# Performance work log

Measured on AMD Instinct MI355X. Metric: run time of the kernel, lower is better.

## Reference

```python
import jax, jax.numpy as jnp
import numpy as np

K = 3
PAD = 1
HEADS = 8
DIM = 256
HEAD_DIM = DIM // HEADS
SCALE = HEAD_DIM ** -0.5
B, IN_C, H, W = 1, 256, 40, 40
DN = ('NCHW', 'OIHW', 'NCHW')


def conv3(x, w):
    return jax.lax.conv_general_dilated(x, w, (1, 1), [(PAD, PAD), (PAD, PAD)], dimension_numbers=DN)


def cbr(x, w, s, b):
    # Conv (no bias) + eval-mode BatchNorm folded into per-channel scale/shift + ReLU
    y = conv3(x, w)
    return jax.nn.relu(y * s[None, :, None, None] + b[None, :, None, None])


def unfold(x):
    # [B,C,H,W] -> [B, C*K*K, H, W]; channels ordered (C, kh, kw), matching torch nn.Unfold
    return jax.lax.conv_general_dilated_patches(x, (K, K), (1, 1), [(PAD, PAD), (PAD, PAD)], dimension_numbers=DN)


def fold(p, h, w):
    # p: [B, C, K, K, h, w]; overlap-add (stride 1), matching F.fold
    b, c = p.shape[:2]
    out = jnp.zeros((b, c, h + 2 * PAD, w + 2 * PAD), p.dtype)
    for i in range(K):
        for j in range(K):
            out = out.at[:, :, i:i + h, j:j + w].add(p[:, :, i, j])
    return out[:, :, PAD:PAD + h, PAD:PAD + w]


def attn_pass(feat_hwc, v_chw, Wa, ba, Wp, bp):
    b, h, w, _ = feat_hwc.shape
    L = h * w
    # unfolded values: [B, heads, L, k^2, head_dim]
    vu = unfold(v_chw).reshape(b, HEADS, HEAD_DIM, K * K, L).transpose(0, 1, 4, 3, 2)
    # attention logits predicted from fg/bg features: [B, heads, L, k^2, k^2]
    logits = (feat_hwc @ Wa + ba).reshape(b, L, HEADS, K * K, K * K).transpose(0, 2, 1, 3, 4) * SCALE
    attn = jax.nn.softmax(logits, axis=-1)
    xw = jnp.einsum('bnlpq,bnlqd->bnlpd', attn, vu)
    # -> [B, dim*k^2, L] layout (C outer, then k^2), reshaped for fold
    xw = xw.transpose(0, 1, 4, 3, 2).reshape(b, DIM, K, K, h, w)
    y = fold(xw, h, w)  # [B, dim, h, w]
    return y.transpose(0, 2, 3, 1) @ Wp + bp  # proj, BHWC


def reference(x, fg, bg, Wc1, s1, b1, Wc2, s2, b2, Wv, bv, Wfg, bfg, Wbg, bbg, Wp, bp, Wc3, s3, b3, Wc4, s4, b4):
    h0 = cbr(cbr(x, Wc1, s1, b1), Wc2, s2, b2)  # input_cbr -> [B, dim, H, W]
    xh = h0.transpose(0, 2, 3, 1)               # BHWC
    v = (xh @ Wv + bv).transpose(0, 3, 1, 2)    # [B, dim, H, W]
    x1 = attn_pass(fg.transpose(0, 2, 3, 1), v, Wfg, bfg, Wp, bp)                            # fg pass, BHWC
    x2 = attn_pass(bg.transpose(0, 2, 3, 1), x1.transpose(0, 3, 1, 2), Wbg, bbg, Wp, bp)     # bg pass, BHWC
    return cbr(cbr(x2.transpose(0, 3, 1, 2), Wc3, s3, b3), Wc4, s4, b4)


def setup_inputs() -> dict:
    key = jax.random.key(0)
    ks = jax.random.split(key, 20)
    def rn(k, shape, s=0.02):
        return jax.random.normal(k, shape, jnp.float32) * s
    A = K ** 4 * HEADS  # 648
    ones = jnp.ones((DIM,), jnp.float32)
    return {
        'x': jax.random.normal(ks[0], (B, IN_C, H, W), jnp.float32),
        'fg': jax.random.normal(ks[1], (B, DIM, H, W), jnp.float32),
        'bg': jax.random.normal(ks[2], (B, DIM, H, W), jnp.float32),
        'Wc1': rn(ks[3], (DIM, IN_C, 3, 3)), 's1': ones, 'b1': rn(ks[4], (DIM,)),
        'Wc2': rn(ks[5], (DIM, DIM, 3, 3)), 's2': ones, 'b2': rn(ks[6], (DIM,)),
        'Wv': rn(ks[7], (DIM, DIM)), 'bv': rn(ks[8], (DIM,)),
        'Wfg': rn(ks[9], (DIM, A)), 'bfg': rn(ks[10], (A,)),
        'Wbg': rn(ks[11], (DIM, A)), 'bbg': rn(ks[12], (A,)),
        'Wp': rn(ks[13], (DIM, DIM)), 'bp': rn(ks[14], (DIM,)),
        'Wc3': rn(ks[15], (DIM, DIM, 3, 3)), 's3': ones, 'b3': rn(ks[16], (DIM,)),
        'Wc4': rn(ks[17], (DIM, DIM, 3, 3)), 's4': ones, 'b4': rn(ks[18], (DIM,)),
    }
```

## Files before the change

kernel.cpp:

```cpp
#include <hip/hip_runtime.h>
#include <hip/hip_bf16.h>

namespace {
constexpr int kHW   = 40;
constexpr int kNPIX = kHW * kHW;
constexpr int kDIM  = 256;
constexpr int kPADW = 42;
constexpr int kACOL = 648;
constexpr float kSCALE = 0.17677669529663687f;
}

using bf16 = __hip_bfloat16;
typedef __attribute__((ext_vector_type(8))) short sh8;
typedef __attribute__((ext_vector_type(4))) float f32x4;

static __device__ __forceinline__ bf16 f2bf(float f)  { return __float2bfloat16(f); }
static __device__ __forceinline__ float bf2f(bf16 b)  { return __bfloat162float(b); }

__global__ __launch_bounds__(256) void prep_all(
    const float* __restrict__ Wc1, const float* __restrict__ Wc2,
    const float* __restrict__ Wc3, const float* __restrict__ Wc4,
    const float* __restrict__ Wfg, const float* __restrict__ Wbg,
    const float* __restrict__ Wv,  const float* __restrict__ Wp,
    const float* __restrict__ x,   const float* __restrict__ fg,
    const float* __restrict__ bg,
    bf16* __restrict__ Wt1, bf16* __restrict__ Wt2,
    bf16* __restrict__ Wt3, bf16* __restrict__ Wt4,
    bf16* __restrict__ WaTf, bf16* __restrict__ WaTb,
    bf16* __restrict__ WvT, bf16* __restrict__ WpT,
    bf16* __restrict__ SHf, bf16* __restrict__ SHb,
    bf16* __restrict__ Pb0, bf16* __restrict__ Pb1) {
  __shared__ float smem[2304];
  int b = blockIdx.x, t = threadIdx.x;

  if (b < 1024) {
    int w = b >> 8, oc = b & 255;
    const float* src = (w == 0) ? Wc1 : (w == 1) ? Wc2 : (w == 2) ? Wc3 : Wc4;
    bf16* dst        = (w == 0) ? Wt1 : (w == 1) ? Wt2 : (w == 2) ? Wt3 : Wt4;
    src += (size_t)oc * 2304;
    for (int i = t; i < 2304; i += 256) smem[i] = src[i];
    __syncthreads();
#pragma unroll
    for (int tap = 0; tap < 9; ++tap)
      dst[(size_t)(tap * 256 + oc) * 256 + t] = f2bf(smem[t * 9 + tap]);
    return;
  }

  float (*tile)[33] = (float(*)[33])smem;
  int tx = t & 31, ty = t >> 5;

  if (b < 1360) {
    int b2 = b - 1024;
    const float* in = (b2 < 168) ? Wfg : Wbg;
    bf16* outp      = (b2 < 168) ? WaTf : WaTb;
    int rb = b2 % 168;
    int bx = rb % 21, by = rb / 21;
    int c0 = bx * 32, r0 = by * 32;
#pragma unroll
    for (int rr = ty; rr < 32; rr += 8) {
      int c = c0 + tx;
      tile[rr][tx] = (c < kACOL) ? in[(size_t)(r0 + rr) * kACOL + c] : 0.f;
    }
    __syncthreads();
#pragma unroll
    for (int rr = ty; rr < 32; rr += 8)
      outp[(size_t)(c0 + rr) * 256 + r0 + tx] = f2bf(tile[tx][rr]);
    return;
  }

  if (b < 1488) {
    int b3 = b - 1360;
    const float* in = (b3 < 64) ? Wv : Wp;
    bf16* outp      = (b3 < 64) ? WvT : WpT;
    int rb = b3 & 63;
    int bx = rb & 7, by = rb >> 3;
    int c0 = bx * 32, r0 = by * 32;
#pragma unroll
    for (int rr = ty; rr < 32; rr += 8)
      tile[rr][tx] = in[(size_t)(r0 + rr) * 256 + c0 + tx];
    __syncthreads();
#pragma unroll
    for (int rr = ty; rr < 32; rr += 8)
      outp[(size_t)(c0 + rr) * 256 + r0 + tx] = f2bf(tile[tx][rr]);
    return;
  }

  if (b < 2288) {
    int b4 = b - 1488;
    const float* in = (b4 < 400) ? fg : bg;
    bf16* outp      = (b4 < 400) ? SHf : SHb;
    int rb = b4 % 400;
    int bx = rb % 50, by = rb / 50;
    int c0 = bx * 32, r0 = by * 32;
#pragma unroll
    for (int rr = ty; rr < 32; rr += 8)
      tile[rr][tx] = in[(size_t)(r0 + rr) * kNPIX + c0 + tx];
    __syncthreads();
#pragma unroll
    for (int rr = ty; rr < 32; rr += 8)
      outp[(size_t)(c0 + rr) * 256 + r0 + tx] = f2bf(tile[tx][rr]);
    return;
  }

  if (b < 2688) {
    int b5 = b - 2288;
    int bx = b5 % 50, by = b5 / 50;
    int c0 = bx * 32, r0 = by * 32;
#pragma unroll
    for (int rr = ty; rr < 32; rr += 8)
      tile[rr][tx] = x[(size_t)(r0 + rr) * kNPIX + c0 + tx];
    __syncthreads();
#pragma unroll
    for (int rr = ty; rr < 32; rr += 8) {
      int l = c0 + rr;
      int yy = l / kHW, xx = l % kHW;
      Pb0[(size_t)((yy + 1) * kPADW + xx + 1) * kDIM + r0 + tx] = f2bf(tile[tx][rr]);
    }
    return;
  }

  {
    int k = b - 2688;
    int py, px;
    if (k < 42)      { py = 0;         px = k; }
    else if (k < 84) { py = 41;        px = k - 42; }
    else if (k < 124){ py = k - 84 + 1; px = 0; }
    else             { py = k - 124 + 1; px = 41; }
    size_t off = (size_t)(py * kPADW + px) * kDIM + t;
    Pb0[off] = f2bf(0.f);
    Pb1[off] = f2bf(0.f);
  }
}

__global__ __launch_bounds__(256) void conv_mfma(const bf16* __restrict__ act,
                                                 const bf16* __restrict__ wt,
                                                 const float* __restrict__ sc,
                                                 const float* __restrict__ sh_,
                                                 bf16* __restrict__ outPad,
                                                 float* __restrict__ outF32) {
  int pt  = blockIdx.x;
  int oc0 = blockIdx.y * 32;
  int ty0 = (pt / 5) * 4;
  int tx0 = (pt % 5) * 8;
  int tid = threadIdx.x;
  int w = tid >> 6, lane = tid & 63, g = lane >> 4, r16 = lane & 15;

  int dy0 = r16 >> 3,       dx0 = r16 & 7;
  int dy1 = 2 + (r16 >> 3), dx1 = r16 & 7;

  f32x4 acc[2][2] = {};
  int icq = w * 64;

#pragma unroll
  for (int t = 0; t < 9; ++t) {
    int tyy = t / 3, txx = t % 3;
    const bf16* aBase0 = act + (size_t)((ty0 + dy0 + tyy) * kPADW + tx0 + dx0 + txx) * kDIM;
    const bf16* aBase1 = act + (size_t)((ty0 + dy1 + tyy) * kPADW + tx0 + dx1 + txx) * kDIM;
    const bf16* bBase  = wt + (size_t)(t * 256 + oc0 + r16) * 256;
#pragma unroll
    for (int kk = 0; kk < 2; ++kk) {
      int ic = icq + kk * 32 + g * 8;
      sh8 a0 = *(const sh8*)(aBase0 + ic);
      sh8 a1 = *(const sh8*)(aBase1 + ic);
      sh8 b0 = *(const sh8*)(bBase + ic);
      sh8 b1 = *(const sh8*)(bBase + 16 * 256 + ic);
      acc[0][0] = __builtin_amdgcn_mfma_f32_16x16x32_bf16(a0, b0, acc[0][0], 0, 0, 0);
      acc[0][1] = __builtin_amdgcn_mfma_f32_16x16x32_bf16(a0, b1, acc[0][1], 0, 0, 0);
      acc[1][0] = __builtin_amdgcn_mfma_f32_16x16x32_bf16(a1, b0, acc[1][0], 0, 0, 0);
      acc[1][1] = __builtin_amdgcn_mfma_f32_16x16x32_bf16(a1, b1, acc[1][1], 0, 0, 0);
    }
  }

  __shared__ float red[4][32][33];
#pragma unroll
  for (int mi = 0; mi < 2; ++mi)
#pragma unroll
    for (int ni = 0; ni < 2; ++ni)
#pragma unroll
      for (int q = 0; q < 4; ++q)
        red[w][mi * 16 + g * 4 + q][ni * 16 + r16] = acc[mi][ni][q];
  __syncthreads();

  int pixL = tid >> 3;
  int ocL  = (tid & 7) * 4;
  int dy = pixL >> 3, dx = pixL & 7;
  int oc = oc0 + ocL;
  int y = ty0 + dy, x = tx0 + dx;
  float v[4];
#pragma unroll
  for (int j = 0; j < 4; ++j) {
    float s = red[0][pixL][ocL + j] + red[1][pixL][ocL + j] +
              red[2][pixL][ocL + j] + red[3][pixL][ocL + j];
    v[j] = fmaxf(fmaf(s, sc[oc + j], sh_[oc + j]), 0.f);
  }
  if (outPad) {
    bf16 pk[4];
#pragma unroll
    for (int j = 0; j < 4; ++j) pk[j] = f2bf(v[j]);
    *reinterpret_cast<uint2*>(outPad + (size_t)((y + 1) * kPADW + x + 1) * kDIM + oc) =
        *reinterpret_cast<uint2*>(pk);
  } else {
#pragma unroll
    for (int j = 0; j < 4; ++j)
      outF32[(oc + j) * kNPIX + y * kHW + x] = v[j];
  }
}

__global__ __launch_bounds__(256) void gemm3_mfma(
    const bf16* __restrict__ Pb0, const bf16* __restrict__ WvT,
    const float* __restrict__ bv, bf16* __restrict__ Vb,
    const bf16* __restrict__ SHf, const bf16* __restrict__ WaTf,
    const float* __restrict__ bfg, bf16* __restrict__ LgF,
    const bf16* __restrict__ SHb, const bf16* __restrict__ WaTb,
    const float* __restrict__ bbg, bf16* __restrict__ LgB) {
  int b = blockIdx.x;
  const bf16 *A, *Bt;
  const float* bias;
  bf16 *oV = nullptr, *oLg = nullptr;
  bool padded = false;
  int l0, col0;
  if (b < 400) {
    padded = true; A = Pb0; Bt = WvT; bias = bv; oV = Vb;
    l0 = (b % 50) * 32; col0 = (b / 50) * 32;
  } else if (b < 1450) {
    int b2 = b - 400;
    A = SHf; Bt = WaTf; bias = bfg; oLg = LgF;
    l0 = (b2 % 50) * 32; col0 = (b2 / 50) * 32;
  } else {
    int b2 = b - 1450;
    A = SHb; Bt = WaTb; bias = bbg; oLg = LgB;
    l0 = (b2 % 50) * 32; col0 = (b2 / 50) * 32;
  }

  int tid = threadIdx.x;
  int w = tid >> 6, lane = tid & 63, g = lane >> 4, r16 = lane & 15;

  const bf16* aBase[2];
#pragma unroll
  for (int mi = 0; mi < 2; ++mi) {
    int l = l0 + mi * 16 + r16;
    if (padded) {
      int y = l / kHW, x = l % kHW;
      aBase[mi] = A + (size_t)((y + 1) * kPADW + x + 1) * kDIM;
    } else {
      aBase[mi] = A + (size_t)l * kDIM;
    }
  }
  const bf16* bBase0 = Bt + (size_t)(col0 + r16) * kDIM;
  const bf16* bBase1 = bBase0 + 16 * kDIM;

  f32x4 acc[2][2] = {};
  int icq = w * 64 + g * 8;
#pragma unroll
  for (int kk = 0; kk < 2; ++kk) {
    int ic = icq + kk * 32;
    sh8 a0 = *(const sh8*)(aBase[0] + ic);
    sh8 a1 = *(const sh8*)(aBase[1] + ic);
    sh8 b0 = *(const sh8*)(bBase0 + ic);
    sh8 b1 = *(const sh8*)(bBase1 + ic);
    acc[0][0] = __builtin_amdgcn_mfma_f32_16x16x32_bf16(a0, b0, acc[0][0], 0, 0, 0);
    acc[0][1] = __builtin_amdgcn_mfma_f32_16x16x32_bf16(a0, b1, acc[0][1], 0, 0, 0);
    acc[1][0] = __builtin_amdgcn_mfma_f32_16x16x32_bf16(a1, b0, acc[1][0], 0, 0, 0);
    acc[1][1] = __builtin_amdgcn_mfma_f32_16x16x32_bf16(a1, b1, acc[1][1], 0, 0, 0);
  }

  __shared__ float red[4][32][33];
#pragma unroll
  for (int mi = 0; mi < 2; ++mi)
#pragma unroll
    for (int ni = 0; ni < 2; ++ni)
#pragma unroll
      for (int q = 0; q < 4; ++q)
        red[w][mi * 16 + g * 4 + q][ni * 16 + r16] = acc[mi][ni][q];
  __syncthreads();

  int pixL = tid >> 3;
  int ocL  = (tid & 7) * 4;
  int l = l0 + pixL;
  int col = col0 + ocL;

  float s[4];
#pragma unroll
  for (int j = 0; j < 4; ++j)
    s[j] = red[0][pixL][ocL + j] + red[1][pixL][ocL + j] +
           red[2][pixL][ocL + j] + red[3][pixL][ocL + j];

  if (oLg) {
#pragma unroll
    for (int j = 0; j < 4; ++j)
      if (col + j < kACOL)
        oLg[(size_t)l * kACOL + col + j] = f2bf((s[j] + bias[col + j]) * kSCALE);
  } else {
    bf16 pk[4];
#pragma unroll
    for (int j = 0; j < 4; ++j) pk[j] = f2bf(s[j] + bias[col + j]);
    *reinterpret_cast<uint2*>(oV + (size_t)l * kDIM + col) =
        *reinterpret_cast<uint2*>(pk);
  }
}

template <int MODE>
__global__ __launch_bounds__(256) void gemm_mfma(const bf16* __restrict__ A,
                                                 const bf16* __restrict__ Bt,
                                                 const float* __restrict__ bias,
                                                 bf16* __restrict__ oBf) {
  int l0   = blockIdx.x * 32;
  int col0 = blockIdx.y * 32;
  int tid = threadIdx.x;
  int w = tid >> 6, lane = tid & 63, g = lane >> 4, r16 = lane & 15;

  const bf16* aBase[2];
#pragma unroll
  for (int mi = 0; mi < 2; ++mi)
    aBase[mi] = A + (size_t)(l0 + mi * 16 + r16) * kDIM;
  const bf16* bBase0 = Bt + (size_t)(col0 + r16) * kDIM;
  const bf16* bBase1 = bBase0 + 16 * kDIM;

  f32x4 acc[2][2] = {};
  int icq = w * 64 + g * 8;
#pragma unroll
  for (int kk = 0; kk < 2; ++kk) {
    int ic = icq + kk * 32;
    sh8 a0 = *(const sh8*)(aBase[0] + ic);
    sh8 a1 = *(const sh8*)(aBase[1] + ic);
    sh8 b0 = *(const sh8*)(bBase0 + ic);
    sh8 b1 = *(const sh8*)(bBase1 + ic);
    acc[0][0] = __builtin_amdgcn_mfma_f32_16x16x32_bf16(a0, b0, acc[0][0], 0, 0, 0);
    acc[0][1] = __builtin_amdgcn_mfma_f32_16x16x32_bf16(a0, b1, acc[0][1], 0, 0, 0);
    acc[1][0] = __builtin_amdgcn_mfma_f32_16x16x32_bf16(a1, b0, acc[1][0], 0, 0, 0);
    acc[1][1] = __builtin_amdgcn_mfma_f32_16x16x32_bf16(a1, b1, acc[1][1], 0, 0, 0);
  }

  __shared__ float red[4][32][33];
#pragma unroll
  for (int mi = 0; mi < 2; ++mi)
#pragma unroll
    for (int ni = 0; ni < 2; ++ni)
#pragma unroll
      for (int q = 0; q < 4; ++q)
        red[w][mi * 16 + g * 4 + q][ni * 16 + r16] = acc[mi][ni][q];
  __syncthreads();

  int pixL = tid >> 3;
  int ocL  = (tid & 7) * 4;
  int l = l0 + pixL;
  int col = col0 + ocL;

  bf16 pk[4];
#pragma unroll
  for (int j = 0; j < 4; ++j) {
    float s = red[0][pixL][ocL + j] + red[1][pixL][ocL + j] +
              red[2][pixL][ocL + j] + red[3][pixL][ocL + j];
    pk[j] = f2bf(s + bias[col + j]);
  }
  if (MODE == 1) {
    *reinterpret_cast<uint2*>(oBf + (size_t)l * kDIM + col) =
        *reinterpret_cast<uint2*>(pk);
  } else {
    int y = l / kHW, x = l % kHW;
    *reinterpret_cast<uint2*>(oBf + (size_t)((y + 1) * kPADW + x + 1) * kDIM + col) =
        *reinterpret_cast<uint2*>(pk);
  }
}

__global__ __launch_bounds__(256) void softmax_pv(const bf16* __restrict__ Lg,
                                                  const bf16* __restrict__ v_hwc,
                                                  bf16* __restrict__ xw) {
  __shared__ float att[kACOL];
  __shared__ float vu[9][kDIM];

  int l = blockIdx.x;
  int y = l / kHW, x = l % kHW;
  int t = threadIdx.x;

#pragma unroll
  for (int r = 0; r < 3; ++r) {
    int a = t + r * 256;
    if (a < kACOL) att[a] = bf2f(Lg[(size_t)l * kACOL + a]);
  }
#pragma unroll
  for (int q = 0; q < 9; ++q) {
    int qy = y + q / 3 - 1;
    int qx = x + q % 3 - 1;
    bool ok = (qy >= 0 && qy < kHW && qx >= 0 && qx < kHW);
    vu[q][t] = ok ? bf2f(v_hwc[(size_t)(qy * kHW + qx) * kDIM + t]) : 0.f;
  }
  __syncthreads();

  if (t < 72) {
    float* gp = &att[t * 9];
    float m = gp[0];
#pragma unroll
    for (int q = 1; q < 9; ++q) m = fmaxf(m, gp[q]);
    float e[9], sm = 0.f;
#pragma unroll
    for (int q = 0; q < 9; ++q) { e[q] = __expf(gp[q] - m); sm += e[q]; }
    float inv = 1.f / sm;
#pragma unroll
    for (int q = 0; q < 9; ++q) gp[q] = e[q] * inv;
  }
  __syncthreads();

  int n = t >> 5;
  const float* an = &att[n * 81];
#pragma unroll
  for (int p = 0; p < 9; ++p) {
    float acc = 0.f;
#pragma unroll
    for (int q = 0; q < 9; ++q)
      acc = fmaf(an[p * 9 + q], vu[q][t], acc);
    xw[(size_t)(l * 9 + p) * kDIM + t] = f2bf(acc);
  }
}

__global__ __launch_bounds__(256) void fold_k(const bf16* __restrict__ xw,
                                              bf16* __restrict__ F) {
  int l = blockIdx.x;
  int Y = l / kHW, X = l % kHW;
  int t = threadIdx.x;
  float acc = 0.f;
#pragma unroll
  for (int i = 0; i < 3; ++i) {
    int ys = Y + 1 - i;
    if (ys < 0 || ys >= kHW) continue;
#pragma unroll
    for (int j = 0; j < 3; ++j) {
      int xs = X + 1 - j;
      if (xs < 0 || xs >= kHW) continue;
      acc += bf2f(xw[(size_t)((ys * kHW + xs) * 9 + i * 3 + j) * kDIM + t]);
    }
  }
  F[(size_t)l * kDIM + t] = f2bf(acc);
}

extern "C" void kernel_launch(void* const* d_in, const int* in_sizes, int n_in,
                              void* d_out, int out_size, void* d_ws, size_t ws_size,
                              hipStream_t stream) {
  const float* x   = (const float*)d_in[0];
  const float* fg  = (const float*)d_in[1];
  const float* bg  = (const float*)d_in[2];
  const float* Wc1 = (const float*)d_in[3];
  const float* s1  = (const float*)d_in[4];
  const float* b1  = (const float*)d_in[5];
  const float* Wc2 = (const float*)d_in[6];
  const float* s2  = (const float*)d_in[7];
  const float* b2  = (const float*)d_in[8];
  const float* Wv  = (const float*)d_in[9];
  const float* bv  = (const float*)d_in[10];
  const float* Wfg = (const float*)d_in[11];
  const float* bfg = (const float*)d_in[12];
  const float* Wbg = (const float*)d_in[13];
  const float* bbg = (const float*)d_in[14];
  const float* Wp  = (const float*)d_in[15];
  const float* bp  = (const float*)d_in[16];
  const float* Wc3 = (const float*)d_in[17];
  const float* s3  = (const float*)d_in[18];
  const float* b3  = (const float*)d_in[19];
  const float* Wc4 = (const float*)d_in[20];
  const float* s4  = (const float*)d_in[21];
  const float* b4  = (const float*)d_in[22];
  float* out = (float*)d_out;

  float* ws = (float*)d_ws;
  bf16* LgF   = (bf16*)ws;
  bf16* LgB   = (bf16*)(ws + 518400);
  bf16* XWb   = (bf16*)(ws + 1036800);
  bf16* SHf   = (bf16*)(ws + 2880000);
  bf16* SHb   = (bf16*)(ws + 3084800);
  bf16* FD    = (bf16*)(ws + 3289600);
  bf16* Vb    = (bf16*)(ws + 3494400);
  bf16* X1b   = (bf16*)(ws + 3699200);
  bf16* Wt1   = (bf16*)(ws + 3904000);
  bf16* Wt2   = Wt1 + 589824;
  bf16* Wt3   = Wt2 + 589824;
  bf16* Wt4   = Wt3 + 589824;
  bf16* WaTf  = (bf16*)(ws + 5083648);
  bf16* WaTb  = (bf16*)(ws + 5169664);
  bf16* WvT   = (bf16*)(ws + 5255680);
  bf16* WpT   = (bf16*)(ws + 5288448);
  bf16* Pb0   = (bf16*)(ws + 5321216);
  bf16* Pb1   = (bf16*)(ws + 5547008);

  prep_all<<<2852, 256, 0, stream>>>(Wc1, Wc2, Wc3, Wc4, Wfg, Wbg, Wv, Wp,
                                     x, fg, bg,
                                     Wt1, Wt2, Wt3, Wt4, WaTf, WaTb, WvT, WpT,
                                     SHf, SHb, Pb0, Pb1);

  const dim3 convGrid(50, 8);
  const dim3 gemmN256(50, 8);

  conv_mfma<<<convGrid, 256, 0, stream>>>(Pb0, Wt1, s1, b1, Pb1, nullptr);
  conv_mfma<<<convGrid, 256, 0, stream>>>(Pb1, Wt2, s2, b2, Pb0, nullptr);

  gemm3_mfma<<<2500, 256, 0, stream>>>(Pb0, WvT, bv, Vb,
                                       SHf, WaTf, bfg, LgF,
                                       SHb, WaTb, bbg, LgB);

  softmax_pv<<<kNPIX, 256, 0, stream>>>(LgF, Vb, XWb);
  fold_k<<<kNPIX, 256, 0, stream>>>(XWb, FD);
  gemm_mfma<1><<<gemmN256, 256, 0, stream>>>(FD, WpT, bp, X1b);

  softmax_pv<<<kNPIX, 256, 0, stream>>>(LgB, X1b, XWb);
  fold_k<<<kNPIX, 256, 0, stream>>>(XWb, FD);
  gemm_mfma<2><<<gemmN256, 256, 0, stream>>>(FD, WpT, bp, Pb1);

  conv_mfma<<<convGrid, 256, 0, stream>>>(Pb1, Wt3, s3, b3, Pb0, nullptr);
  conv_mfma<<<convGrid, 256, 0, stream>>>(Pb0, Wt4, s4, b4, nullptr, out);
}
```

Before: 131.3 us.

## Fuse fold overlap-add into projection GEMM via shared-memory tile

```diff
diff --git a/kernel.cpp b/kernel.cpp
--- a/kernel.cpp
+++ b/kernel.cpp
@@ -16,6 +16,11 @@
 
 static __device__ __forceinline__ bf16 f2bf(float f)  { return __float2bfloat16(f); }
 static __device__ __forceinline__ float bf2f(bf16 b)  { return __bfloat162float(b); }
+static __device__ __forceinline__ float sraw2f(short s) {
+  union { unsigned int u; float f; } c;
+  c.u = ((unsigned int)(unsigned short)s) << 16;
+  return c.f;
+}
 
 __global__ __launch_bounds__(256) void prep_all(
     const float* __restrict__ Wc1, const float* __restrict__ Wc2,
@@ -300,66 +305,71 @@
 }
 
 template <int MODE>
-__global__ __launch_bounds__(256) void gemm_mfma(const bf16* __restrict__ A,
-                                                 const bf16* __restrict__ Bt,
-                                                 const float* __restrict__ bias,
-                                                 bf16* __restrict__ oBf) {
-  int l0   = blockIdx.x * 32;
-  int col0 = blockIdx.y * 32;
+__global__ __launch_bounds__(512) void foldproj_mfma(const bf16* __restrict__ xw,
+                                                     const bf16* __restrict__ Bt,
+                                                     const float* __restrict__ bias,
+                                                     bf16* __restrict__ oBf) {
+  __shared__ bf16 fold_s[16][264];
+  int l0 = blockIdx.x * 16;
   int tid = threadIdx.x;
+
+  {
+    int s  = tid >> 5;
+    int cb = (tid & 31) * 8;
+    int l = l0 + s;
+    int Y = l / kHW, X = l % kHW;
+    float facc[8] = {};
+#pragma unroll
+    for (int i = 0; i < 3; ++i) {
+      int ys = Y + 1 - i;
+      if (ys < 0 || ys >= kHW) continue;
+#pragma unroll
+      for (int j = 0; j < 3; ++j) {
+        int xs = X + 1 - j;
+        if (xs < 0 || xs >= kHW) continue;
+        sh8 v = *(const sh8*)(xw + (size_t)((ys * kHW + xs) * 9 + i * 3 + j) * kDIM + cb);
+#pragma unroll
+        for (int e = 0; e < 8; ++e) facc[e] += sraw2f(v[e]);
+      }
+    }
+    bf16 pk[8];
+#pragma unroll
+    for (int e = 0; e < 8; ++e) pk[e] = f2bf(facc[e]);
+    *reinterpret_cast<sh8*>(&fold_s[s][cb]) = *reinterpret_cast<sh8*>(pk);
+  }
+  __syncthreads();
+
   int w = tid >> 6, lane = tid & 63, g = lane >> 4, r16 = lane & 15;
-
-  const bf16* aBase[2];
-#pragma unroll
-  for (int mi = 0; mi < 2; ++mi)
-    aBase[mi] = A + (size_t)(l0 + mi * 16 + r16) * kDIM;
+  int col0 = w * 32;
   const bf16* bBase0 = Bt + (size_t)(col0 + r16) * kDIM;
   const bf16* bBase1 = bBase0 + 16 * kDIM;
 
-  f32x4 acc[2][2] = {};
-  int icq = w * 64 + g * 8;
-#pragma unroll
-  for (int kk = 0; kk < 2; ++kk) {
-    int ic = icq + kk * 32;
-    sh8 a0 = *(const sh8*)(aBase[0] + ic);
-    sh8 a1 = *(const sh8*)(aBase[1] + ic);
-    sh8 b0 = *(const sh8*)(bBase0 + ic);
-    sh8 b1 = *(const sh8*)(bBase1 + ic);
-    acc[0][0] = __builtin_amdgcn_mfma_f32_16x16x32_bf16(a0, b0, acc[0][0], 0, 0, 0);
-    acc[0][1] = __builtin_amdgcn_mfma_f32_16x16x32_bf16(a0, b1, acc[0][1], 0, 0, 0);
-    acc[1][0] = __builtin_amdgcn_mfma_f32_16x16x32_bf16(a1, b0, acc[1][0], 0, 0, 0);
-    acc[1][1] = __builtin_amdgcn_mfma_f32_16x16x32_bf16(a1, b1, acc[1][1], 0, 0, 0);
-  }
-
-  __shared__ float red[4][32][33];
-#pragma unroll
-  for (int mi = 0; mi < 2; ++mi)
-#pragma unroll
-    for (int ni = 0; ni < 2; ++ni)
-#pragma unroll
-      for (int q = 0; q < 4; ++q)
-        red[w][mi * 16 + g * 4 + q][ni * 16 + r16] = acc[mi][ni][q];
-  __syncthreads();
-
-  int pixL = tid >> 3;
-  int ocL  = (tid & 7) * 4;
-  int l = l0 + pixL;
-  int col = col0 + ocL;
-
-  bf16 pk[4];
-#pragma unroll
-  for (int j = 0; j < 4; ++j) {
-    float s = red[0][pixL][ocL + j] + red[1][pixL][ocL + j] +
-              red[2][pixL][ocL + j] + red[3][pixL][ocL + j];
-    pk[j] = f2bf(s + bias[col + j]);
-  }
-  if (MODE == 1) {
-    *reinterpret_cast<uint2*>(oBf + (size_t)l * kDIM + col) =
-        *reinterpret_cast<uint2*>(pk);
-  } else {
-    int y = l / kHW, x = l % kHW;
-    *reinterpret_cast<uint2*>(oBf + (size_t)((y + 1) * kPADW + x + 1) * kDIM + col) =
-        *reinterpret_cast<uint2*>(pk);
+  f32x4 acc[2] = {};
+#pragma unroll
+  for (int kk = 0; kk < 8; ++kk) {
+    int k = kk * 32 + g * 8;
+    sh8 a  = *(const sh8*)(&fold_s[r16][k]);
+    sh8 b0 = *(const sh8*)(bBase0 + k);
+    sh8 b1 = *(const sh8*)(bBase1 + k);
+    acc[0] = __builtin_amdgcn_mfma_f32_16x16x32_bf16(a, b0, acc[0], 0, 0, 0);
+    acc[1] = __builtin_amdgcn_mfma_f32_16x16x32_bf16(a, b1, acc[1], 0, 0, 0);
+  }
+
+#pragma unroll
+  for (int ni = 0; ni < 2; ++ni) {
+    int col = col0 + ni * 16 + r16;
+    float bb = bias[col];
+#pragma unroll
+    for (int q = 0; q < 4; ++q) {
+      int l = l0 + g * 4 + q;
+      bf16 val = f2bf(acc[ni][q] + bb);
+      if (MODE == 1) {
+        oBf[(size_t)l * kDIM + col] = val;
+      } else {
+        int y = l / kHW, xx = l % kHW;
+        oBf[(size_t)((y + 1) * kPADW + xx + 1) * kDIM + col] = val;
+      }
+    }
   }
 }
 
@@ -411,26 +421,6 @@
       acc = fmaf(an[p * 9 + q], vu[q][t], acc);
     xw[(size_t)(l * 9 + p) * kDIM + t] = f2bf(acc);
   }
-}
-
-__global__ __launch_bounds__(256) void fold_k(const bf16* __restrict__ xw,
-                                              bf16* __restrict__ F) {
-  int l = blockIdx.x;
-  int Y = l / kHW, X = l % kHW;
-  int t = threadIdx.x;
-  float acc = 0.f;
-#pragma unroll
-  for (int i = 0; i < 3; ++i) {
-    int ys = Y + 1 - i;
-    if (ys < 0 || ys >= kHW) continue;
-#pragma unroll
-    for (int j = 0; j < 3; ++j) {
-      int xs = X + 1 - j;
-      if (xs < 0 || xs >= kHW) continue;
-      acc += bf2f(xw[(size_t)((ys * kHW + xs) * 9 + i * 3 + j) * kDIM + t]);
-    }
-  }
-  F[(size_t)l * kDIM + t] = f2bf(acc);
 }
 
 extern "C" void kernel_launch(void* const* d_in, const int* in_sizes, int n_in,
@@ -467,7 +457,6 @@
   bf16* XWb   = (bf16*)(ws + 1036800);
   bf16* SHf   = (bf16*)(ws + 2880000);
   bf16* SHb   = (bf16*)(ws + 3084800);
-  bf16* FD    = (bf16*)(ws + 3289600);
   bf16* Vb    = (bf16*)(ws + 3494400);
   bf16* X1b   = (bf16*)(ws + 3699200);
   bf16* Wt1   = (bf16*)(ws + 3904000);
@@ -487,7 +476,6 @@
                                      SHf, SHb, Pb0, Pb1);
 
   const dim3 convGrid(50, 8);
-  const dim3 gemmN256(50, 8);
 
   conv_mfma<<<convGrid, 256, 0, stream>>>(Pb0, Wt1, s1, b1, Pb1, nullptr);
   conv_mfma<<<convGrid, 256, 0, stream>>>(Pb1, Wt2, s2, b2, Pb0, nullptr);
@@ -497,12 +485,10 @@
                                        SHb, WaTb, bbg, LgB);
 
   softmax_pv<<<kNPIX, 256, 0, stream>>>(LgF, Vb, XWb);
-  fold_k<<<kNPIX, 256, 0, stream>>>(XWb, FD);
-  gemm_mfma<1><<<gemmN256, 256, 0, stream>>>(FD, WpT, bp, X1b);
+  foldproj_mfma<1><<<100, 512, 0, stream>>>(XWb, WpT, bp, X1b);
 
   softmax_pv<<<kNPIX, 256, 0, stream>>>(LgB, X1b, XWb);
-  fold_k<<<kNPIX, 256, 0, stream>>>(XWb, FD);
-  gemm_mfma<2><<<gemmN256, 256, 0, stream>>>(FD, WpT, bp, Pb1);
+  foldproj_mfma<2><<<100, 512, 0, stream>>>(XWb, WpT, bp, Pb1);
 
   conv_mfma<<<convGrid, 256, 0, stream>>>(Pb1, Wt3, s3, b3, Pb0, nullptr);
   conv_mfma<<<convGrid, 256, 0, stream>>>(Pb0, Wt4, s4, b4, nullptr, out);
```

New measurement: 132.2 us. About the same (+0.6%).
